# Kernel optimization log

Hardware: AMD Instinct MI355X
Metric: run time of the kernel (lower is better)

## Reference

```python
import jax, jax.numpy as jnp
import numpy as np

HEADS = 4
DIM_HEAD = 32
SCALE = DIM_HEAD ** -0.5
EPS = 1e-5


def setup_inputs() -> dict:
    key = jax.random.key(0)
    ks = jax.random.split(key, 4)
    B, C, H, W = 16, 128, 32, 32
    hid = HEADS * DIM_HEAD  # 128
    return {
        "x": jax.random.normal(ks[0], (B, C, H, W), jnp.float32),
        "gn_weight": jnp.ones((C,), jnp.float32),
        "gn_bias": jnp.zeros((C,), jnp.float32),
        "w_qkv": jax.random.normal(ks[1], (3 * hid, C), jnp.float32) * 0.05,  # 1x1 conv, no bias
        "w_out": jax.random.normal(ks[2], (C, hid), jnp.float32) * 0.05,      # 1x1 conv
        "b_out": jax.random.normal(ks[3], (C,), jnp.float32) * 0.05,
    }


def reference(x, gn_weight, gn_bias, w_qkv, w_out, b_out):
    B, C, H, W = x.shape
    N = H * W
    # GroupNorm(num_groups=1): normalize over (C, H, W) per sample, per-channel affine
    mu = x.mean(axis=(1, 2, 3), keepdims=True)
    var = x.var(axis=(1, 2, 3), keepdims=True)
    xn = (x - mu) * jax.lax.rsqrt(var + EPS)
    xn = xn * gn_weight[None, :, None, None] + gn_bias[None, :, None, None]

    xf = xn.reshape(B, C, N)  # b c n
    qkv = jnp.einsum('bcn,oc->bon', xf, w_qkv)  # 1x1 conv == matmul over channels
    q, k, v = jnp.split(qkv, 3, axis=1)

    def to_heads(t):  # 'b (h c) x y -> b h (x y) c'
        return t.reshape(B, HEADS, DIM_HEAD, N).transpose(0, 1, 3, 2)  # b h n c

    q, k, v = map(to_heads, (q, k, v))

    q = jax.nn.softmax(q, axis=-2) * SCALE  # softmax over spatial tokens
    k = jax.nn.softmax(k, axis=-1)          # softmax over channel dim

    # Faithful to source einsums: contract over CHANNEL dim -> (b, h, N, N) context
    context = jnp.einsum('bhdc,bhec->bhde', k, v)      # b h n n
    out = jnp.einsum('bhde,bhdc->bhec', context, q)    # b h n c

    # 'b h (x y) c -> b (h c) x y'
    outf = out.transpose(0, 1, 3, 2).reshape(B, HEADS * DIM_HEAD, N)
    y = jnp.einsum('bcn,oc->bon', outf, w_out) + b_out[None, :, None]
    return y.reshape(B, C, H, W)
```

## Files before the change

kernel.cpp:

```cpp
#include <hip/hip_runtime.h>
#include <math.h>

#define CIN 128
#define NTOK 1024
#define SCALE_Q 0.17677669529663687f
#define GN_EPS 1e-5f
#define PB (CIN * NTOK)

#define WS_WQKVB 0
#define WS_PSTATS 24576
#define WS_PQSUM 25088
#define WS_VST 57856
#define WS_PM 1106432

typedef __bf16 bf16x8 __attribute__((ext_vector_type(8)));
typedef float f32x4 __attribute__((ext_vector_type(4)));

__device__ __forceinline__ unsigned short f2bf(float f) {
    union { float f; unsigned u; } v; v.f = f;
    unsigned r = v.u + 0x7fffu + ((v.u >> 16) & 1u);
    return (unsigned short)(r >> 16);
}
__device__ __forceinline__ unsigned pack2(float a, float b) {
    return (unsigned)f2bf(a) | ((unsigned)f2bf(b) << 16);
}

__global__ __launch_bounds__(256) void k_pre(const float* __restrict__ x,
                                             const float* __restrict__ wqkv,
                                             float* __restrict__ ws) {
    float* pstats = ws + WS_PSTATS;
    unsigned short* wqkvb = (unsigned short*)(ws + WS_WQKVB);
    __shared__ float sD[8];
    int bid = blockIdx.x, t = threadIdx.x;
    int lane = t & 63, wave = t >> 6;
    const float4* p = (const float4*)(x + (size_t)bid * 8192);
    float s = 0.f, s2 = 0.f;
    #pragma unroll
    for (int i = 0; i < 8; i++) {
        float4 v = p[t + 256 * i];
        s += v.x + v.y + v.z + v.w;
        s2 += v.x * v.x + v.y * v.y + v.z * v.z + v.w * v.w;
    }
    #pragma unroll
    for (int off = 32; off; off >>= 1) {
        s += __shfl_down(s, off);
        s2 += __shfl_down(s2, off);
    }
    if (lane == 0) { sD[wave * 2] = s; sD[wave * 2 + 1] = s2; }
    if (bid < 48) {
        float4 v = ((const float4*)(wqkv + bid * 1024))[t];
        uint2 pk2; pk2.x = pack2(v.x, v.y); pk2.y = pack2(v.z, v.w);
        *(uint2*)(wqkvb + bid * 1024 + t * 4) = pk2;
    }
    __syncthreads();
    if (t == 0) {
        pstats[bid * 2] = sD[0] + sD[2] + sD[4] + sD[6];
        pstats[bid * 2 + 1] = sD[1] + sD[3] + sD[5] + sD[7];
    }
}

__global__ __launch_bounds__(512, 1) void k_qkvm(const float* __restrict__ x,
                                                 const float* __restrict__ gw,
                                                 const float* __restrict__ gb,
                                                 float* __restrict__ ws) {
    __shared__ __align__(16) char smem[124928];
    unsigned short (*Al)[136] = (unsigned short(*)[136])smem;
    unsigned short (*Bl)[136] = (unsigned short(*)[136])(smem + 17408);
    float (*Xl)[68] = (float(*)[68])(smem + 17408);
    unsigned short (*kTl)[72] = (unsigned short(*)[72])(smem + 87040);
    unsigned short (*Vl)[136] = (unsigned short(*)[136])(smem + 87040);
    unsigned short (*qTl)[72] = (unsigned short(*)[72])(smem + 105472);
    float* sD = (float*)(smem + 123904);

    unsigned short* wqkvb = (unsigned short*)(ws + WS_WQKVB);
    float* pstats = ws + WS_PSTATS;
    float* pqsum = ws + WS_PQSUM;
    unsigned short* Vst = (unsigned short*)(ws + WS_VST);
    float* pM = ws + WS_PM;

    int bid = blockIdx.x, t = threadIdx.x;
    int b = bid >> 4, nt = bid & 15;
    int lane = t & 63, wave = t >> 6;
    int l15 = lane & 15, lk = (lane >> 4) * 8;
    int sel = wave >> 1;
    int wn0 = (wave & 1) * 32;

    if (t < 32) sD[t] = pstats[b * 32 + t];
    __syncthreads();
    float mu, rsv;
    {
        float s = 0.f, s2 = 0.f;
        #pragma unroll
        for (int i = 0; i < 16; i++) { s += sD[2 * i]; s2 += sD[2 * i + 1]; }
        mu = s * (1.f / PB);
        float var = s2 * (1.f / PB) - mu * mu;
        rsv = rsqrtf(var + GN_EPS);
    }
    {
        int c = t >> 2, qtr = t & 3;
        float g = gw[c] * rsv, bb = gb[c] - mu * g;
        const float4* src = (const float4*)(x + ((size_t)b * CIN + c) * NTOK + nt * 64 + qtr * 16);
        #pragma unroll
        for (int i = 0; i < 4; i++) {
            float4 v = src[i];
            float4 r = { v.x * g + bb, v.y * g + bb, v.z * g + bb, v.w * g + bb };
            *(float4*)&Xl[c][qtr * 16 + i * 4] = r;
        }
    }
    __syncthreads();
    {
        int n = t & 63, kq = (t >> 6) * 16;
        unsigned pk[8];
        #pragma unroll
        for (int j = 0; j < 8; j++) pk[j] = pack2(Xl[kq + 2 * j][n], Xl[kq + 2 * j + 1][n]);
        *(uint4*)&Al[n][kq] = *(uint4*)pk;
        *(uint4*)(&Al[n][kq] + 8) = *(uint4*)(pk + 4);
    }
    __syncthreads();
    {
        int row = t >> 1, hf = t & 1;
        const uint4* src = (const uint4*)(wqkvb + (size_t)row * CIN + hf * 64);
        uint4* dst = (uint4*)&Bl[row][hf * 64];
        #pragma unroll
        for (int j = 0; j < 8; j++) dst[j] = src[j];
    }
    __syncthreads();

    f32x4 acc[2][4] = {};
    #pragma unroll
    for (int ks = 0; ks < 4; ks++) {
        bf16x8 av[2], bv[4];
        #pragma unroll
        for (int i = 0; i < 2; i++) av[i] = *(const bf16x8*)&Al[wn0 + i * 16 + l15][ks * 32 + lk];
        #pragma unroll
        for (int j = 0; j < 4; j++) bv[j] = *(const bf16x8*)&Bl[sel * 64 + j * 16 + l15][ks * 32 + lk];
        #pragma unroll
        for (int i = 0; i < 2; i++)
            #pragma unroll
            for (int j = 0; j < 4; j++)
                acc[i][j] = __builtin_amdgcn_mfma_f32_16x16x32_bf16(av[i], bv[j], acc[i][j], 0, 0, 0);
    }

    float e[2][4][4];
    #pragma unroll
    for (int i = 0; i < 2; i++)
        #pragma unroll
        for (int j = 0; j < 4; j++)
            #pragma unroll
            for (int r = 0; r < 4; r++) e[i][j][r] = __expf(acc[i][j][r]);

    if (sel >= 2) {
        #pragma unroll
        for (int i = 0; i < 2; i++)
            #pragma unroll
            for (int r = 0; r < 4; r++) {
                float e01 = e[i][0][r] + e[i][1][r];
                float e23 = e[i][2][r] + e[i][3][r];
                #pragma unroll
                for (int m = 1; m < 16; m <<= 1) {
                    e01 += __shfl_xor(e01, m);
                    e23 += __shfl_xor(e23, m);
                }
                float i01 = 1.f / e01, i23 = 1.f / e23;
                e[i][0][r] *= i01; e[i][1][r] *= i01;
                e[i][2][r] *= i23; e[i][3][r] *= i23;
            }
        #pragma unroll
        for (int i = 0; i < 2; i++)
            #pragma unroll
            for (int j = 0; j < 4; j++) {
                int ch = (sel - 2) * 64 + j * 16 + l15;
                int tokb = wn0 + i * 16 + (lane >> 4) * 4;
                *(unsigned*)&kTl[ch][tokb] = pack2(e[i][j][0], e[i][j][1]);
                *(unsigned*)&kTl[ch][tokb + 2] = pack2(e[i][j][2], e[i][j][3]);
            }
    } else {
        #pragma unroll
        for (int i = 0; i < 2; i++)
            #pragma unroll
            for (int j = 0; j < 4; j++) {
                int ch = sel * 64 + j * 16 + l15;
                int tokb = wn0 + i * 16 + (lane >> 4) * 4;
                *(unsigned*)&qTl[ch][tokb] = pack2(e[i][j][0], e[i][j][1]);
                *(unsigned*)&qTl[ch][tokb + 2] = pack2(e[i][j][2], e[i][j][3]);
            }
        #pragma unroll
        for (int j = 0; j < 4; j++) {
            float sq = 0.f;
            #pragma unroll
            for (int i = 0; i < 2; i++)
                #pragma unroll
                for (int r = 0; r < 4; r++) sq += e[i][j][r];
            sq += __shfl_xor(sq, 16);
            sq += __shfl_xor(sq, 32);
            if (lane < 16) sD[(wave & 1) * 128 + sel * 64 + j * 16 + lane] = sq;
        }
    }
    __syncthreads();
    if (t < 128) pqsum[(size_t)bid * 128 + t] = sD[t] + sD[128 + t];

    if (wave < 4) {
        int h = wave;
        f32x4 mac[2][2] = {};
        #pragma unroll
        for (int ks = 0; ks < 2; ks++) {
            bf16x8 av[2], bv[2];
            #pragma unroll
            for (int i = 0; i < 2; i++) av[i] = *(const bf16x8*)&kTl[h * 32 + i * 16 + l15][ks * 32 + lk];
            #pragma unroll
            for (int j = 0; j < 2; j++) bv[j] = *(const bf16x8*)&qTl[h * 32 + j * 16 + l15][ks * 32 + lk];
            #pragma unroll
            for (int i = 0; i < 2; i++)
                #pragma unroll
                for (int j = 0; j < 2; j++)
                    mac[i][j] = __builtin_amdgcn_mfma_f32_16x16x32_bf16(av[i], bv[j], mac[i][j], 0, 0, 0);
        }
        float* pmb = pM + ((size_t)bid * 4 + h) * 1024;
        #pragma unroll
        for (int i = 0; i < 2; i++)
            #pragma unroll
            for (int j = 0; j < 2; j++)
                #pragma unroll
                for (int r = 0; r < 4; r++)
                    pmb[(i * 16 + (lane >> 4) * 4 + r) * 32 + j * 16 + l15] = mac[i][j][r];
    } else {
        int t2 = t - 256;
        int row = t2 >> 1, hf = t2 & 1;
        const uint4* src = (const uint4*)(wqkvb + (size_t)(256 + row) * CIN + hf * 64);
        uint4* dst = (uint4*)&Bl[row][hf * 64];
        #pragma unroll
        for (int j = 0; j < 8; j++) dst[j] = src[j];
    }
    __syncthreads();

    {
        int wo0v = sel * 32;
        f32x4 vacc[2][2] = {};
        #pragma unroll
        for (int ks = 0; ks < 4; ks++) {
            bf16x8 av[2], bv[2];
            #pragma unroll
            for (int i = 0; i < 2; i++) av[i] = *(const bf16x8*)&Al[wn0 + i * 16 + l15][ks * 32 + lk];
            #pragma unroll
            for (int j = 0; j < 2; j++) bv[j] = *(const bf16x8*)&Bl[wo0v + j * 16 + l15][ks * 32 + lk];
            #pragma unroll
            for (int i = 0; i < 2; i++)
                #pragma unroll
                for (int j = 0; j < 2; j++)
                    vacc[i][j] = __builtin_amdgcn_mfma_f32_16x16x32_bf16(av[i], bv[j], vacc[i][j], 0, 0, 0);
        }
        #pragma unroll
        for (int i = 0; i < 2; i++)
            #pragma unroll
            for (int j = 0; j < 2; j++) {
                int ch = wo0v + j * 16 + l15;
                #pragma unroll
                for (int r = 0; r < 4; r++)
                    Vl[wn0 + i * 16 + (lane >> 4) * 4 + r][ch] = f2bf(vacc[i][j][r]);
            }
    }
    __syncthreads();
    {
        int row = t >> 3, qq = t & 7;
        uint4* dst = (uint4*)(Vst + ((size_t)bid * 64 + row) * CIN + qq * 16);
        dst[0] = *(uint4*)&Vl[row][qq * 16];
        dst[1] = *(uint4*)&Vl[row][qq * 16 + 8];
    }
}

__global__ __launch_bounds__(512, 1) void k_out(const float* __restrict__ wout,
                                                const float* __restrict__ bout,
                                                float* __restrict__ ws,
                                                float* __restrict__ y) {
    __shared__ __align__(16) char smem[80384];
    unsigned short (*Wl)[136] = (unsigned short(*)[136])smem;
    unsigned short (*Ul)[136] = (unsigned short(*)[136])(smem + 34816);
    unsigned short (*Vl)[136] = (unsigned short(*)[136])(smem + 52224);
    unsigned short (*Mt)[32][40] = (unsigned short(*)[32][40])(smem + 69632);
    float* sD = (float*)(smem + 79872);

    float* pqsum = ws + WS_PQSUM;
    unsigned short* Vst = (unsigned short*)(ws + WS_VST);
    float* pM = ws + WS_PM;

    int bid = blockIdx.x, t = threadIdx.x;
    int b = bid >> 4, nt = bid & 15;
    int lane = t & 63, wave = t >> 6;
    int l15 = lane & 15, lk = (lane >> 4) * 8;
    int wn0 = (wave & 1) * 32;

    if (t < 128) {
        float s = 0.f;
        #pragma unroll
        for (int i = 0; i < 16; i++) s += pqsum[((size_t)(b * 16 + i)) * 128 + t];
        sD[t] = SCALE_Q / s;
    }
    {
        int row = t >> 3, qq = t & 7;
        const uint4* src = (const uint4*)(Vst + ((size_t)bid * 64 + row) * CIN + qq * 16);
        *(uint4*)&Vl[row][qq * 16] = src[0];
        *(uint4*)&Vl[row][qq * 16 + 8] = src[1];
    }
    #pragma unroll
    for (int s4 = 0; s4 < 2; s4++) {
        int slot = t + (s4 << 9);
        int h = slot >> 8, cp = (slot >> 3) & 31, c4 = slot & 7;
        float4 m = { 0.f, 0.f, 0.f, 0.f };
        for (int i = 0; i < 16; i++) {
            const float4 v = *(const float4*)&pM[(((size_t)(b * 16 + i)) * 4 + h) * 1024 + cp * 32 + c4 * 4];
            m.x += v.x; m.y += v.y; m.z += v.z; m.w += v.w;
        }
        Mt[h][c4 * 4 + 0][cp] = f2bf(m.x);
        Mt[h][c4 * 4 + 1][cp] = f2bf(m.y);
        Mt[h][c4 * 4 + 2][cp] = f2bf(m.z);
        Mt[h][c4 * 4 + 3][cp] = f2bf(m.w);
    }
    __syncthreads();

    int head = wave >> 1;
    f32x4 uac[2][2] = {};
    {
        bf16x8 mv[2];
        #pragma unroll
        for (int j = 0; j < 2; j++) mv[j] = *(const bf16x8*)&Mt[head][j * 16 + l15][lk];
        #pragma unroll
        for (int i = 0; i < 2; i++) {
            bf16x8 av = *(const bf16x8*)&Vl[wn0 + i * 16 + l15][head * 32 + lk];
            #pragma unroll
            for (int j = 0; j < 2; j++)
                uac[i][j] = __builtin_amdgcn_mfma_f32_16x16x32_bf16(av, mv[j], uac[i][j], 0, 0, 0);
        }
    }
    {
        int o = t >> 2, qtr = t & 3;
        const float4* src = (const float4*)(wout + (size_t)o * CIN + qtr * 32);
        unsigned pk[16];
        #pragma unroll
        for (int i = 0; i < 8; i++) {
            float4 v = src[i];
            int c = qtr * 32 + i * 4;
            v.x *= sD[c]; v.y *= sD[c + 1]; v.z *= sD[c + 2]; v.w *= sD[c + 3];
            pk[2 * i] = pack2(v.x, v.y);
            pk[2 * i + 1] = pack2(v.z, v.w);
        }
        uint4* dst = (uint4*)&Wl[o][qtr * 32];
        #pragma unroll
        for (int j = 0; j < 4; j++) dst[j] = *(uint4*)(pk + j * 4);
    }
    #pragma unroll
    for (int i = 0; i < 2; i++)
        #pragma unroll
        for (int j = 0; j < 2; j++) {
            int ch = head * 32 + j * 16 + l15;
            #pragma unroll
            for (int r = 0; r < 4; r++)
                Ul[wn0 + i * 16 + (lane >> 4) * 4 + r][ch] = f2bf(uac[i][j][r]);
        }
    __syncthreads();

    int wo0 = (wave >> 1) * 32;
    f32x4 yacc[2][2] = {};
    #pragma unroll
    for (int ks = 0; ks < 4; ks++) {
        bf16x8 av[2], bv[2];
        #pragma unroll
        for (int i = 0; i < 2; i++) av[i] = *(const bf16x8*)&Wl[wo0 + i * 16 + l15][ks * 32 + lk];
        #pragma unroll
        for (int j = 0; j < 2; j++) bv[j] = *(const bf16x8*)&Ul[wn0 + j * 16 + l15][ks * 32 + lk];
        #pragma unroll
        for (int i = 0; i < 2; i++)
            #pragma unroll
            for (int j = 0; j < 2; j++)
                yacc[i][j] = __builtin_amdgcn_mfma_f32_16x16x32_bf16(av[i], bv[j], yacc[i][j], 0, 0, 0);
    }
    #pragma unroll
    for (int i = 0; i < 2; i++)
        #pragma unroll
        for (int r = 0; r < 4; r++) {
            int o = wo0 + i * 16 + (lane >> 4) * 4 + r;
            float bias = bout[o];
            float* yp = y + ((size_t)b * CIN + o) * NTOK + nt * 64 + wn0;
            #pragma unroll
            for (int j = 0; j < 2; j++) yp[j * 16 + l15] = yacc[i][j][r] + bias;
        }
}

extern "C" void kernel_launch(void* const* d_in, const int* in_sizes, int n_in,
                              void* d_out, int out_size, void* d_ws, size_t ws_size,
                              hipStream_t stream) {
    const float* x = (const float*)d_in[0];
    const float* gw = (const float*)d_in[1];
    const float* gb = (const float*)d_in[2];
    const float* wqkv = (const float*)d_in[3];
    const float* wout = (const float*)d_in[4];
    const float* bout = (const float*)d_in[5];
    float* y = (float*)d_out;
    float* ws = (float*)d_ws;

    k_pre<<<dim3(256), 256, 0, stream>>>(x, wqkv, ws);
    k_qkvm<<<dim3(256), 512, 0, stream>>>(x, gw, gb, ws);
    k_out<<<dim3(256), 512, 0, stream>>>(wout, bout, ws, y);
}
```

Before: 92.90 us.

## Fold V projection, context and output conv into per-batch effective weight

The V projection, the per-head context application and the output 1x1 conv are reassociated into one per-batch 128x128 effective weight, with GroupNorm scale and shift and the q-softmax normalisation folded in. A small 16-block kernel builds this weight and a per-batch bias. The final kernel then does a single GEMM of the raw input against it. This drops the V-staging round trip through global memory and the extra per-tile MFMA stages, but adds a fourth launch and a low-parallelism 16-block kernel on the critical path, plus extra bf16 rounding of the composed weight.

```diff
diff --git a/kernel.cpp b/kernel.cpp
--- a/kernel.cpp
+++ b/kernel.cpp
@@ -8,10 +8,12 @@
 #define PB (CIN * NTOK)
 
 #define WS_WQKVB 0
+#define WS_WVT   16384
 #define WS_PSTATS 24576
 #define WS_PQSUM 25088
-#define WS_VST 57856
-#define WS_PM 1106432
+#define WS_PMT   57856
+#define WS_WEFF  1106432
+#define WS_BIAS  1237504
 
 typedef __bf16 bf16x8 __attribute__((ext_vector_type(8)));
 typedef float f32x4 __attribute__((ext_vector_type(4)));
@@ -30,6 +32,7 @@
                                              float* __restrict__ ws) {
     float* pstats = ws + WS_PSTATS;
     unsigned short* wqkvb = (unsigned short*)(ws + WS_WQKVB);
+    unsigned short* wvT = (unsigned short*)(ws + WS_WVT);
     __shared__ float sD[8];
     int bid = blockIdx.x, t = threadIdx.x;
     int lane = t & 63, wave = t >> 6;
@@ -47,10 +50,19 @@
         s2 += __shfl_down(s2, off);
     }
     if (lane == 0) { sD[wave * 2] = s; sD[wave * 2 + 1] = s2; }
-    if (bid < 48) {
+    if (bid < 32) {
         float4 v = ((const float4*)(wqkv + bid * 1024))[t];
         uint2 pk2; pk2.x = pack2(v.x, v.y); pk2.y = pack2(v.z, v.w);
         *(uint2*)(wqkvb + bid * 1024 + t * 4) = pk2;
+    } else if (bid < 48) {
+        int g = bid - 32;
+        int kk = g * 8 + (t >> 5), cq = t & 31;
+        float v0 = wqkv[(256 + cq * 4 + 0) * 128 + kk];
+        float v1 = wqkv[(256 + cq * 4 + 1) * 128 + kk];
+        float v2 = wqkv[(256 + cq * 4 + 2) * 128 + kk];
+        float v3 = wqkv[(256 + cq * 4 + 3) * 128 + kk];
+        uint2 pk2; pk2.x = pack2(v0, v1); pk2.y = pack2(v2, v3);
+        *(uint2*)(wvT + kk * 128 + cq * 4) = pk2;
     }
     __syncthreads();
     if (t == 0) {
@@ -59,24 +71,22 @@
     }
 }
 
-__global__ __launch_bounds__(512, 1) void k_qkvm(const float* __restrict__ x,
-                                                 const float* __restrict__ gw,
-                                                 const float* __restrict__ gb,
-                                                 float* __restrict__ ws) {
-    __shared__ __align__(16) char smem[124928];
+__global__ __launch_bounds__(512, 1) void k_qk(const float* __restrict__ x,
+                                               const float* __restrict__ gw,
+                                               const float* __restrict__ gb,
+                                               float* __restrict__ ws) {
+    __shared__ __align__(16) char smem[122880];
     unsigned short (*Al)[136] = (unsigned short(*)[136])smem;
-    unsigned short (*Bl)[136] = (unsigned short(*)[136])(smem + 17408);
     float (*Xl)[68] = (float(*)[68])(smem + 17408);
-    unsigned short (*kTl)[72] = (unsigned short(*)[72])(smem + 87040);
-    unsigned short (*Vl)[136] = (unsigned short(*)[136])(smem + 87040);
-    unsigned short (*qTl)[72] = (unsigned short(*)[72])(smem + 105472);
-    float* sD = (float*)(smem + 123904);
+    unsigned short (*kTl)[68] = (unsigned short(*)[68])(smem + 17408);
+    unsigned short (*qTl)[68] = (unsigned short(*)[68])(smem + 34816);
+    unsigned short (*Bl)[136] = (unsigned short(*)[136])(smem + 52224);
+    float* sD = (float*)(smem + 121856);
 
     unsigned short* wqkvb = (unsigned short*)(ws + WS_WQKVB);
     float* pstats = ws + WS_PSTATS;
     float* pqsum = ws + WS_PQSUM;
-    unsigned short* Vst = (unsigned short*)(ws + WS_VST);
-    float* pM = ws + WS_PM;
+    float* pMT = ws + WS_PMT;
 
     int bid = blockIdx.x, t = threadIdx.x;
     int b = bid >> 4, nt = bid & 15;
@@ -86,6 +96,16 @@
     int wn0 = (wave & 1) * 32;
 
     if (t < 32) sD[t] = pstats[b * 32 + t];
+    int cx = t >> 2, qtr = t & 3;
+    const float4* xsrc = (const float4*)(x + ((size_t)b * CIN + cx) * NTOK + nt * 64 + qtr * 16);
+    float4 xr0 = xsrc[0], xr1 = xsrc[1], xr2 = xsrc[2], xr3 = xsrc[3];
+    {
+        int row = t >> 1, hf = t & 1;
+        const uint4* src = (const uint4*)(wqkvb + (size_t)row * CIN + hf * 64);
+        uint4* dst = (uint4*)&Bl[row][hf * 64];
+        #pragma unroll
+        for (int j = 0; j < 8; j++) dst[j] = src[j];
+    }
     __syncthreads();
     float mu, rsv;
     {
@@ -97,15 +117,15 @@
         rsv = rsqrtf(var + GN_EPS);
     }
     {
-        int c = t >> 2, qtr = t & 3;
-        float g = gw[c] * rsv, bb = gb[c] - mu * g;
-        const float4* src = (const float4*)(x + ((size_t)b * CIN + c) * NTOK + nt * 64 + qtr * 16);
-        #pragma unroll
-        for (int i = 0; i < 4; i++) {
-            float4 v = src[i];
-            float4 r = { v.x * g + bb, v.y * g + bb, v.z * g + bb, v.w * g + bb };
-            *(float4*)&Xl[c][qtr * 16 + i * 4] = r;
-        }
+        float g = gw[cx] * rsv, bb = gb[cx] - mu * g;
+        float4 r0 = { xr0.x * g + bb, xr0.y * g + bb, xr0.z * g + bb, xr0.w * g + bb };
+        float4 r1 = { xr1.x * g + bb, xr1.y * g + bb, xr1.z * g + bb, xr1.w * g + bb };
+        float4 r2 = { xr2.x * g + bb, xr2.y * g + bb, xr2.z * g + bb, xr2.w * g + bb };
+        float4 r3 = { xr3.x * g + bb, xr3.y * g + bb, xr3.z * g + bb, xr3.w * g + bb };
+        *(float4*)&Xl[cx][qtr * 16 + 0] = r0;
+        *(float4*)&Xl[cx][qtr * 16 + 4] = r1;
+        *(float4*)&Xl[cx][qtr * 16 + 8] = r2;
+        *(float4*)&Xl[cx][qtr * 16 + 12] = r3;
     }
     __syncthreads();
     {
@@ -117,15 +137,6 @@
         *(uint4*)(&Al[n][kq] + 8) = *(uint4*)(pk + 4);
     }
     __syncthreads();
-    {
-        int row = t >> 1, hf = t & 1;
-        const uint4* src = (const uint4*)(wqkvb + (size_t)row * CIN + hf * 64);
-        uint4* dst = (uint4*)&Bl[row][hf * 64];
-        #pragma unroll
-        for (int j = 0; j < 8; j++) dst[j] = src[j];
-    }
-    __syncthreads();
-
     f32x4 acc[2][4] = {};
     #pragma unroll
     for (int ks = 0; ks < 4; ks++) {
@@ -140,7 +151,6 @@
             for (int j = 0; j < 4; j++)
                 acc[i][j] = __builtin_amdgcn_mfma_f32_16x16x32_bf16(av[i], bv[j], acc[i][j], 0, 0, 0);
     }
-
     float e[2][4][4];
     #pragma unroll
     for (int i = 0; i < 2; i++)
@@ -198,7 +208,6 @@
     }
     __syncthreads();
     if (t < 128) pqsum[(size_t)bid * 128 + t] = sD[t] + sD[128 + t];
-
     if (wave < 4) {
         int h = wave;
         f32x4 mac[2][2] = {};
@@ -206,16 +215,16 @@
         for (int ks = 0; ks < 2; ks++) {
             bf16x8 av[2], bv[2];
             #pragma unroll
-            for (int i = 0; i < 2; i++) av[i] = *(const bf16x8*)&kTl[h * 32 + i * 16 + l15][ks * 32 + lk];
-            #pragma unroll
-            for (int j = 0; j < 2; j++) bv[j] = *(const bf16x8*)&qTl[h * 32 + j * 16 + l15][ks * 32 + lk];
+            for (int i = 0; i < 2; i++) av[i] = *(const bf16x8*)&qTl[h * 32 + i * 16 + l15][ks * 32 + lk];
+            #pragma unroll
+            for (int j = 0; j < 2; j++) bv[j] = *(const bf16x8*)&kTl[h * 32 + j * 16 + l15][ks * 32 + lk];
             #pragma unroll
             for (int i = 0; i < 2; i++)
                 #pragma unroll
                 for (int j = 0; j < 2; j++)
                     mac[i][j] = __builtin_amdgcn_mfma_f32_16x16x32_bf16(av[i], bv[j], mac[i][j], 0, 0, 0);
         }
-        float* pmb = pM + ((size_t)bid * 4 + h) * 1024;
+        float* pmb = pMT + ((size_t)bid * 4 + h) * 1024;
         #pragma unroll
         for (int i = 0; i < 2; i++)
             #pragma unroll
@@ -223,165 +232,216 @@
                 #pragma unroll
                 for (int r = 0; r < 4; r++)
                     pmb[(i * 16 + (lane >> 4) * 4 + r) * 32 + j * 16 + l15] = mac[i][j][r];
-    } else {
-        int t2 = t - 256;
-        int row = t2 >> 1, hf = t2 & 1;
-        const uint4* src = (const uint4*)(wqkvb + (size_t)(256 + row) * CIN + hf * 64);
-        uint4* dst = (uint4*)&Bl[row][hf * 64];
-        #pragma unroll
-        for (int j = 0; j < 8; j++) dst[j] = src[j];
-    }
-    __syncthreads();
-
-    {
-        int wo0v = sel * 32;
-        f32x4 vacc[2][2] = {};
-        #pragma unroll
-        for (int ks = 0; ks < 4; ks++) {
-            bf16x8 av[2], bv[2];
-            #pragma unroll
-            for (int i = 0; i < 2; i++) av[i] = *(const bf16x8*)&Al[wn0 + i * 16 + l15][ks * 32 + lk];
-            #pragma unroll
-            for (int j = 0; j < 2; j++) bv[j] = *(const bf16x8*)&Bl[wo0v + j * 16 + l15][ks * 32 + lk];
-            #pragma unroll
-            for (int i = 0; i < 2; i++)
-                #pragma unroll
-                for (int j = 0; j < 2; j++)
-                    vacc[i][j] = __builtin_amdgcn_mfma_f32_16x16x32_bf16(av[i], bv[j], vacc[i][j], 0, 0, 0);
-        }
-        #pragma unroll
-        for (int i = 0; i < 2; i++)
-            #pragma unroll
-            for (int j = 0; j < 2; j++) {
-                int ch = wo0v + j * 16 + l15;
-                #pragma unroll
-                for (int r = 0; r < 4; r++)
-                    Vl[wn0 + i * 16 + (lane >> 4) * 4 + r][ch] = f2bf(vacc[i][j][r]);
-            }
-    }
-    __syncthreads();
-    {
-        int row = t >> 3, qq = t & 7;
-        uint4* dst = (uint4*)(Vst + ((size_t)bid * 64 + row) * CIN + qq * 16);
-        dst[0] = *(uint4*)&Vl[row][qq * 16];
-        dst[1] = *(uint4*)&Vl[row][qq * 16 + 8];
-    }
-}
-
-__global__ __launch_bounds__(512, 1) void k_out(const float* __restrict__ wout,
-                                                const float* __restrict__ bout,
-                                                float* __restrict__ ws,
-                                                float* __restrict__ y) {
-    __shared__ __align__(16) char smem[80384];
-    unsigned short (*Wl)[136] = (unsigned short(*)[136])smem;
-    unsigned short (*Ul)[136] = (unsigned short(*)[136])(smem + 34816);
-    unsigned short (*Vl)[136] = (unsigned short(*)[136])(smem + 52224);
-    unsigned short (*Mt)[32][40] = (unsigned short(*)[32][40])(smem + 69632);
-    float* sD = (float*)(smem + 79872);
-
+    }
+}
+
+__global__ __launch_bounds__(512, 1) void k_weff(const float* __restrict__ gw,
+                                                 const float* __restrict__ gb,
+                                                 const float* __restrict__ wout,
+                                                 const float* __restrict__ bout,
+                                                 float* __restrict__ ws) {
+    __shared__ __align__(16) char smem[116736];
+    unsigned short (*pMTb)[32][40] = (unsigned short(*)[32][40])smem;
+    unsigned short (*wvTb)[136] = (unsigned short(*)[136])(smem + 10240);
+    unsigned short (*WeffL)[136] = (unsigned short(*)[136])(smem + 10240);
+    unsigned short (*woutb)[136] = (unsigned short(*)[136])(smem + 45056);
+    unsigned short (*B2T)[136] = (unsigned short(*)[136])(smem + 79872);
+    float* sD = (float*)(smem + 114688);
+
+    float* pstats = ws + WS_PSTATS;
     float* pqsum = ws + WS_PQSUM;
-    unsigned short* Vst = (unsigned short*)(ws + WS_VST);
-    float* pM = ws + WS_PM;
-
-    int bid = blockIdx.x, t = threadIdx.x;
-    int b = bid >> 4, nt = bid & 15;
+    float* pMT = ws + WS_PMT;
+    unsigned short* wvT = (unsigned short*)(ws + WS_WVT);
+    unsigned short* weffg = (unsigned short*)(ws + WS_WEFF);
+    float* biasg = ws + WS_BIAS;
+
+    int b = blockIdx.x, t = threadIdx.x;
     int lane = t & 63, wave = t >> 6;
     int l15 = lane & 15, lk = (lane >> 4) * 8;
-    int wn0 = (wave & 1) * 32;
-
+
+    if (t < 32) sD[384 + t] = pstats[b * 32 + t];
     if (t < 128) {
         float s = 0.f;
         #pragma unroll
-        for (int i = 0; i < 16; i++) s += pqsum[((size_t)(b * 16 + i)) * 128 + t];
+        for (int i = 0; i < 16; i++) s += pqsum[(size_t)(b * 16 + i) * 128 + t];
         sD[t] = SCALE_Q / s;
     }
-    {
-        int row = t >> 3, qq = t & 7;
-        const uint4* src = (const uint4*)(Vst + ((size_t)bid * 64 + row) * CIN + qq * 16);
-        *(uint4*)&Vl[row][qq * 16] = src[0];
-        *(uint4*)&Vl[row][qq * 16 + 8] = src[1];
-    }
-    #pragma unroll
-    for (int s4 = 0; s4 < 2; s4++) {
-        int slot = t + (s4 << 9);
-        int h = slot >> 8, cp = (slot >> 3) & 31, c4 = slot & 7;
+    #pragma unroll
+    for (int s2 = 0; s2 < 2; s2++) {
+        int f4 = t * 2 + s2;
+        int h = f4 >> 8, c = (f4 >> 3) & 31, cp0 = (f4 & 7) * 4;
         float4 m = { 0.f, 0.f, 0.f, 0.f };
         for (int i = 0; i < 16; i++) {
-            const float4 v = *(const float4*)&pM[(((size_t)(b * 16 + i)) * 4 + h) * 1024 + cp * 32 + c4 * 4];
+            float4 v = *(const float4*)&pMT[(((size_t)(b * 16 + i)) * 4 + h) * 1024 + c * 32 + cp0];
             m.x += v.x; m.y += v.y; m.z += v.z; m.w += v.w;
         }
-        Mt[h][c4 * 4 + 0][cp] = f2bf(m.x);
-        Mt[h][c4 * 4 + 1][cp] = f2bf(m.y);
-        Mt[h][c4 * 4 + 2][cp] = f2bf(m.z);
-        Mt[h][c4 * 4 + 3][cp] = f2bf(m.w);
-    }
-    __syncthreads();
-
-    int head = wave >> 1;
-    f32x4 uac[2][2] = {};
-    {
-        bf16x8 mv[2];
-        #pragma unroll
-        for (int j = 0; j < 2; j++) mv[j] = *(const bf16x8*)&Mt[head][j * 16 + l15][lk];
-        #pragma unroll
-        for (int i = 0; i < 2; i++) {
-            bf16x8 av = *(const bf16x8*)&Vl[wn0 + i * 16 + l15][head * 32 + lk];
-            #pragma unroll
-            for (int j = 0; j < 2; j++)
-                uac[i][j] = __builtin_amdgcn_mfma_f32_16x16x32_bf16(av, mv[j], uac[i][j], 0, 0, 0);
-        }
-    }
-    {
-        int o = t >> 2, qtr = t & 3;
-        const float4* src = (const float4*)(wout + (size_t)o * CIN + qtr * 32);
-        unsigned pk[16];
+        uint2 u; u.x = pack2(m.x, m.y); u.y = pack2(m.z, m.w);
+        *(uint2*)&pMTb[h][c][cp0] = u;
+    }
+    {
+        int row = t >> 2, q4 = t & 3;
+        const uint4* src = (const uint4*)(wvT + row * 128) + q4 * 4;
+        #pragma unroll
+        for (int m = 0; m < 4; m++) *(uint4*)&wvTb[row][q4 * 32 + m * 8] = src[m];
+    }
+    {
+        int row = t >> 2, q4 = t & 3;
+        const float4* src = (const float4*)(wout + row * 128 + q4 * 32);
         #pragma unroll
         for (int i = 0; i < 8; i++) {
             float4 v = src[i];
-            int c = qtr * 32 + i * 4;
-            v.x *= sD[c]; v.y *= sD[c + 1]; v.z *= sD[c + 2]; v.w *= sD[c + 3];
-            pk[2 * i] = pack2(v.x, v.y);
-            pk[2 * i + 1] = pack2(v.z, v.w);
-        }
-        uint4* dst = (uint4*)&Wl[o][qtr * 32];
-        #pragma unroll
-        for (int j = 0; j < 4; j++) dst[j] = *(uint4*)(pk + j * 4);
-    }
-    #pragma unroll
-    for (int i = 0; i < 2; i++)
-        #pragma unroll
-        for (int j = 0; j < 2; j++) {
-            int ch = head * 32 + j * 16 + l15;
-            #pragma unroll
-            for (int r = 0; r < 4; r++)
-                Ul[wn0 + i * 16 + (lane >> 4) * 4 + r][ch] = f2bf(uac[i][j][r]);
-        }
-    __syncthreads();
-
-    int wo0 = (wave >> 1) * 32;
-    f32x4 yacc[2][2] = {};
+            uint2 u; u.x = pack2(v.x, v.y); u.y = pack2(v.z, v.w);
+            *(uint2*)&woutb[row][q4 * 32 + i * 4] = u;
+        }
+    }
+    __syncthreads();
+    if (t < 128) {
+        float s = 0.f, s2 = 0.f;
+        #pragma unroll
+        for (int i = 0; i < 16; i++) { s += sD[384 + 2 * i]; s2 += sD[384 + 2 * i + 1]; }
+        float mu = s * (1.f / PB);
+        float var = s2 * (1.f / PB) - mu * mu;
+        float rs = rsqrtf(var + GN_EPS);
+        float gsc = gw[t] * rs;
+        sD[128 + t] = gsc;
+        sD[256 + t] = gb[t] - mu * gsc;
+    }
+    __syncthreads();
+    {
+        int h = wave >> 1, kh = wave & 1;
+        f32x4 mac[2][4] = {};
+        bf16x8 av[2];
+        #pragma unroll
+        for (int i = 0; i < 2; i++) av[i] = *(const bf16x8*)&pMTb[h][i * 16 + l15][lk];
+        #pragma unroll
+        for (int j = 0; j < 4; j++) {
+            bf16x8 bv = *(const bf16x8*)&wvTb[kh * 64 + j * 16 + l15][h * 32 + lk];
+            #pragma unroll
+            for (int i = 0; i < 2; i++)
+                mac[i][j] = __builtin_amdgcn_mfma_f32_16x16x32_bf16(av[i], bv, mac[i][j], 0, 0, 0);
+        }
+        #pragma unroll
+        for (int i = 0; i < 2; i++)
+            #pragma unroll
+            for (int j = 0; j < 4; j++) {
+                int k = kh * 64 + j * 16 + l15;
+                int cb = h * 32 + i * 16 + (lane >> 4) * 4;
+                float q0 = sD[cb], q1 = sD[cb + 1], q2 = sD[cb + 2], q3 = sD[cb + 3];
+                uint2 u;
+                u.x = pack2(mac[i][j][0] * q0, mac[i][j][1] * q1);
+                u.y = pack2(mac[i][j][2] * q2, mac[i][j][3] * q3);
+                *(uint2*)&B2T[k][cb] = u;
+            }
+    }
+    __syncthreads();
+    {
+        f32x4 acc[8] = {};
+        #pragma unroll
+        for (int ks = 0; ks < 4; ks++) {
+            bf16x8 av = *(const bf16x8*)&woutb[wave * 16 + l15][ks * 32 + lk];
+            #pragma unroll
+            for (int j = 0; j < 8; j++) {
+                bf16x8 bv = *(const bf16x8*)&B2T[j * 16 + l15][ks * 32 + lk];
+                acc[j] = __builtin_amdgcn_mfma_f32_16x16x32_bf16(av, bv, acc[j], 0, 0, 0);
+            }
+        }
+        float gs[8], bbv[8];
+        #pragma unroll
+        for (int j = 0; j < 8; j++) {
+            int k = j * 16 + l15;
+            gs[j] = sD[128 + k];
+            bbv[j] = sD[256 + k];
+        }
+        #pragma unroll
+        for (int r = 0; r < 4; r++) {
+            int o = wave * 16 + (lane >> 4) * 4 + r;
+            float pb = 0.f;
+            #pragma unroll
+            for (int j = 0; j < 8; j++) {
+                float wv = acc[j][r];
+                pb += wv * bbv[j];
+                WeffL[o][j * 16 + l15] = f2bf(wv * gs[j]);
+            }
+            pb += __shfl_xor(pb, 1);
+            pb += __shfl_xor(pb, 2);
+            pb += __shfl_xor(pb, 4);
+            pb += __shfl_xor(pb, 8);
+            if (l15 == 0) biasg[b * 128 + o] = bout[o] + pb;
+        }
+    }
+    __syncthreads();
+    {
+        int row = t >> 2, q4 = t & 3;
+        #pragma unroll
+        for (int m = 0; m < 4; m++)
+            *(uint4*)(weffg + (size_t)b * 16384 + row * 128 + q4 * 32 + m * 8) =
+                *(uint4*)&WeffL[row][q4 * 32 + m * 8];
+    }
+}
+
+__global__ __launch_bounds__(512, 1) void k_out2(const float* __restrict__ x,
+                                                 float* __restrict__ ws,
+                                                 float* __restrict__ y) {
+    __shared__ __align__(16) char smem[87552];
+    unsigned short (*Wfb)[136] = (unsigned short(*)[136])smem;
+    float (*Xl)[68] = (float(*)[68])(smem + 34816);
+    unsigned short (*xT)[136] = (unsigned short(*)[136])(smem + 69632);
+    float* sDb = (float*)(smem + 87040);
+
+    unsigned short* weffg = (unsigned short*)(ws + WS_WEFF);
+    float* biasg = ws + WS_BIAS;
+
+    int nt = blockIdx.x, b = blockIdx.y, t = threadIdx.x;
+    int lane = t & 63, wave = t >> 6;
+    int l15 = lane & 15, lk = (lane >> 4) * 8;
+
+    if (t < 128) sDb[t] = biasg[b * 128 + t];
+    {
+        int row = t >> 2, q4 = t & 3;
+        const uint4* src = (const uint4*)(weffg + (size_t)b * 16384 + row * 128) + q4 * 4;
+        #pragma unroll
+        for (int m = 0; m < 4; m++) *(uint4*)&Wfb[row][q4 * 32 + m * 8] = src[m];
+    }
+    {
+        int cx = t >> 2, qtr = t & 3;
+        const float4* xsrc = (const float4*)(x + ((size_t)b * CIN + cx) * NTOK + nt * 64 + qtr * 16);
+        #pragma unroll
+        for (int i = 0; i < 4; i++) *(float4*)&Xl[cx][qtr * 16 + i * 4] = xsrc[i];
+    }
+    __syncthreads();
+    {
+        int n = t & 63, kq = (t >> 6) * 16;
+        unsigned pk[8];
+        #pragma unroll
+        for (int j = 0; j < 8; j++) pk[j] = pack2(Xl[kq + 2 * j][n], Xl[kq + 2 * j + 1][n]);
+        *(uint4*)&xT[n][kq] = *(uint4*)pk;
+        *(uint4*)(&xT[n][kq] + 8) = *(uint4*)(pk + 4);
+    }
+    __syncthreads();
+    int o0 = (wave >> 1) * 32, n0 = (wave & 1) * 32;
+    f32x4 acc[2][2] = {};
     #pragma unroll
     for (int ks = 0; ks < 4; ks++) {
         bf16x8 av[2], bv[2];
         #pragma unroll
-        for (int i = 0; i < 2; i++) av[i] = *(const bf16x8*)&Wl[wo0 + i * 16 + l15][ks * 32 + lk];
-        #pragma unroll
-        for (int j = 0; j < 2; j++) bv[j] = *(const bf16x8*)&Ul[wn0 + j * 16 + l15][ks * 32 + lk];
+        for (int i = 0; i < 2; i++) av[i] = *(const bf16x8*)&Wfb[o0 + i * 16 + l15][ks * 32 + lk];
+        #pragma unroll
+        for (int j = 0; j < 2; j++) bv[j] = *(const bf16x8*)&xT[n0 + j * 16 + l15][ks * 32 + lk];
         #pragma unroll
         for (int i = 0; i < 2; i++)
             #pragma unroll
             for (int j = 0; j < 2; j++)
-                yacc[i][j] = __builtin_amdgcn_mfma_f32_16x16x32_bf16(av[i], bv[j], yacc[i][j], 0, 0, 0);
+                acc[i][j] = __builtin_amdgcn_mfma_f32_16x16x32_bf16(av[i], bv[j], acc[i][j], 0, 0, 0);
     }
     #pragma unroll
     for (int i = 0; i < 2; i++)
         #pragma unroll
         for (int r = 0; r < 4; r++) {
-            int o = wo0 + i * 16 + (lane >> 4) * 4 + r;
-            float bias = bout[o];
-            float* yp = y + ((size_t)b * CIN + o) * NTOK + nt * 64 + wn0;
-            #pragma unroll
-            for (int j = 0; j < 2; j++) yp[j * 16 + l15] = yacc[i][j][r] + bias;
+            int o = o0 + i * 16 + (lane >> 4) * 4 + r;
+            float bias = sDb[o];
+            float* yp = y + ((size_t)b * CIN + o) * NTOK + nt * 64 + n0;
+            #pragma unroll
+            for (int j = 0; j < 2; j++) yp[j * 16 + l15] = acc[i][j][r] + bias;
         }
 }
 
@@ -398,6 +458,7 @@
     float* ws = (float*)d_ws;
 
     k_pre<<<dim3(256), 256, 0, stream>>>(x, wqkv, ws);
-    k_qkvm<<<dim3(256), 512, 0, stream>>>(x, gw, gb, ws);
-    k_out<<<dim3(256), 512, 0, stream>>>(wout, bout, ws, y);
-}
+    k_qk<<<dim3(256), 512, 0, stream>>>(x, gw, gb, ws);
+    k_weff<<<dim3(16), 512, 0, stream>>>(gw, gb, wout, bout, ws);
+    k_out2<<<dim3(16, 16), 512, 0, stream>>>(x, ws, y);
+}
```

Measured after the change: 97.63 us. +5.1%, slower.
